# Optimization experiments

Measured on AMD Instinct MI355X. Metric: run time of the kernel, lower is better.

The kernel has to match this reference:

```python
import jax, jax.numpy as jnp
import numpy as np

NEG_POS_RATIO = 3
LOC_LOSS_ALPHA = 1.0
B, N, C = 64, 8732, 21  # batch, total prior boxes (SSD300), classes (VOC)


def setup_inputs() -> dict:
    key = jax.random.key(0)
    kd, km, kl, kpd, kpl = jax.random.split(key, 5)
    pos_mask = jax.random.bernoulli(km, 0.02, (B, N))
    actual_bbox_deltas = jax.random.normal(kd, (B, N, 4), dtype=jnp.float32) * pos_mask[..., None]
    cls = jax.random.randint(kl, (B, N), 0, C)
    actual_labels = jax.nn.one_hot(cls, C, dtype=jnp.float32)
    pred_bbox_deltas = jax.random.normal(kpd, (B, N, 4), dtype=jnp.float32)
    pred_labels = jax.random.normal(kpl, (B, N, C), dtype=jnp.float32)
    return {
        "actual_bbox_deltas": actual_bbox_deltas,
        "actual_labels": actual_labels,
        "pred_bbox_deltas": pred_bbox_deltas,
        "pred_labels": pred_labels,
    }


def reference(actual_bbox_deltas, actual_labels, pred_bbox_deltas, pred_labels):
    # positive boxes: any nonzero delta
    pos_cond = jnp.any(actual_bbox_deltas != 0, axis=2)          # [B, N] bool
    pos_count = jnp.sum(pos_cond, axis=1)                         # [B]
    neg_count = pos_count * NEG_POS_RATIO                         # [B]

    # CE from logits, used only to rank negatives for hard-negative mining
    ce_logits = -jnp.sum(actual_labels * jax.nn.log_softmax(pred_labels, axis=-1), axis=-1)  # [B, N]
    masked_loss = jnp.where(pos_cond, -jnp.inf, ce_logits)
    # rank[b, n] = position of box n in descending sort of masked_loss[b]
    order = jnp.argsort(-masked_loss, axis=1)
    rank = jnp.argsort(order, axis=1)
    neg_mask = rank < neg_count[:, None]                          # hardest negatives
    sel_mask = pos_cond | neg_mask                                # boxes entering conf loss

    total_pos = jnp.maximum(jnp.sum(pos_count), 1).astype(jnp.float32)

    # Huber (delta=1): TF Huber takes mean over last axis, then reduction='sum'
    d = pred_bbox_deltas - actual_bbox_deltas
    ad = jnp.abs(d)
    hub = jnp.where(ad <= 1.0, 0.5 * d * d, ad - 0.5)             # [B, N, 4]
    loc_loss = jnp.sum(jnp.mean(hub, axis=-1) * pos_cond) * LOC_LOSS_ALPHA

    # conf loss: TF CategoricalCrossentropy with from_logits=False (as in the original code,
    # applied to the raw pred_labels): normalize to sum 1, clip to epsilon, -sum(y*log p)
    eps = 1e-7
    p = pred_labels / jnp.sum(pred_labels, axis=-1, keepdims=True)
    p = jnp.clip(p, eps, 1.0 - eps)
    ce_probs = -jnp.sum(actual_labels * jnp.log(p), axis=-1)      # [B, N]
    conf_loss = jnp.sum(ce_probs * sel_mask)

    return loc_loss / total_pos, conf_loss / total_pos
```

## Files before the change

kernel.cpp:

```cpp
#include <hip/hip_runtime.h>
#include <math.h>

#define BB 64
#define NN 8732
#define NV4 (NN / 4)
#define CC 21
#define TB 256
#define GX 35

static __device__ __forceinline__ unsigned f2u(float f) {
  unsigned u = __float_as_uint(f);
  return (u & 0x80000000u) ? ~u : (u | 0x80000000u);
}

__global__ __launch_bounds__(256) void k1_map(
    const float* __restrict__ abd, const float* __restrict__ lbl,
    const float* __restrict__ pbd, const float* __restrict__ plog,
    unsigned* __restrict__ keys, float* __restrict__ cep,
    float* __restrict__ pl, float* __restrict__ pc, int* __restrict__ pcnt) {
  __shared__ float s_plog[TB * CC];
  __shared__ int s_cls[TB];
  __shared__ float s_l[4], s_p[4];
  __shared__ int s_c[4];

  const int b = blockIdx.y;
  const int base = blockIdx.x * TB;
  const int nbox = min(TB, NN - base);
  const int nf4 = (nbox * CC) / 4;
  const int tid = threadIdx.x;

  const float4* pl4 = reinterpret_cast<const float4*>(plog + ((size_t)b * NN + base) * CC);
  for (int t = tid; t < nf4; t += 256) {
    reinterpret_cast<float4*>(s_plog)[t] = pl4[t];
  }
  const float4* lb4 = reinterpret_cast<const float4*>(lbl + ((size_t)b * NN + base) * CC);
  for (int t = tid; t < nf4; t += 256) {
    float4 v = lb4[t];
    const unsigned f0 = (unsigned)t * 4u;
    if (v.x != 0.f) s_cls[(f0 + 0) / CC] = (int)((f0 + 0) % CC);
    if (v.y != 0.f) s_cls[(f0 + 1) / CC] = (int)((f0 + 1) % CC);
    if (v.z != 0.f) s_cls[(f0 + 2) / CC] = (int)((f0 + 2) % CC);
    if (v.w != 0.f) s_cls[(f0 + 3) / CC] = (int)((f0 + 3) % CC);
  }
  __syncthreads();

  const int n = base + tid;
  const bool valid = (tid < nbox);
  float loc = 0.f, pconf = 0.f;
  int isPos = 0;
  if (valid) {
    const size_t idx = (size_t)b * NN + n;
    const float4 a = reinterpret_cast<const float4*>(abd)[idx];
    const float4 p = reinterpret_cast<const float4*>(pbd)[idx];
    isPos = (a.x != 0.f) || (a.y != 0.f) || (a.z != 0.f) || (a.w != 0.f);

    const int cls = s_cls[tid];
    float pv[CC];
    float m = -INFINITY, ssum = 0.f, tdot = 0.f;
#pragma unroll
    for (int j = 0; j < CC; ++j) {
      const float v = s_plog[tid * CC + j];
      pv[j] = v;
      m = fmaxf(m, v);
      ssum += v;
      tdot = (j == cls) ? v : tdot;
    }
    float es = 0.f;
#pragma unroll
    for (int j = 0; j < CC; ++j) es += expf(pv[j] - m);
    float pt = tdot / ssum;
    float ptc = fminf(fmaxf(pt, 1e-7f), 1.0f - 1e-7f);
    float cp = -logf(ptc);
    float cel = (m + logf(es)) - tdot;
    keys[idx] = isPos ? 0u : f2u(cel);
    cep[idx] = cp;
    pconf = isPos ? cp : 0.f;
    float dx = p.x - a.x, dy = p.y - a.y, dz = p.z - a.z, dw = p.w - a.w;
    float axv = fabsf(dx), ayv = fabsf(dy), azv = fabsf(dz), awv = fabsf(dw);
    float h = (axv <= 1.f ? 0.5f * dx * dx : axv - 0.5f)
            + (ayv <= 1.f ? 0.5f * dy * dy : ayv - 0.5f)
            + (azv <= 1.f ? 0.5f * dz * dz : azv - 0.5f)
            + (awv <= 1.f ? 0.5f * dw * dw : awv - 0.5f);
    loc = isPos ? h * 0.25f : 0.f;
  }
  float lv = loc, pcf = pconf;
  int pctr = isPos;
  for (int off = 32; off > 0; off >>= 1) {
    lv += __shfl_down(lv, off, 64);
    pcf += __shfl_down(pcf, off, 64);
    pctr += __shfl_down(pctr, off, 64);
  }
  const int lane = tid & 63, wv = tid >> 6;
  if (lane == 0) { s_l[wv] = lv; s_p[wv] = pcf; s_c[wv] = pctr; }
  __syncthreads();
  if (tid == 0) {
    const int bi = b * GX + blockIdx.x;
    pl[bi] = s_l[0] + s_l[1] + s_l[2] + s_l[3];
    pc[bi] = s_p[0] + s_p[1] + s_p[2] + s_p[3];
    pcnt[bi] = s_c[0] + s_c[1] + s_c[2] + s_c[3];
  }
}

#define K2T 1024
#define K2W 16

__global__ __launch_bounds__(K2T) void k2_select(
    const unsigned* __restrict__ keys, const float* __restrict__ cep,
    const float* __restrict__ pl, const float* __restrict__ pc,
    const int* __restrict__ pcnt,
    double* __restrict__ row_loc, double* __restrict__ row_conf,
    int* __restrict__ row_pos) {
  __shared__ unsigned hist[2048];
  __shared__ unsigned wsum[K2W];
  __shared__ unsigned bc[2];
  __shared__ unsigned wtot[K2W];
  __shared__ double s_d[K2W];
  __shared__ double s_rl, s_rc;
  __shared__ int s_pos;
  const int b = blockIdx.x;
  const int tid = threadIdx.x;
  const int lane = tid & 63, wv = tid >> 6;

  if (wv == 0) {
    float a = 0.f, c = 0.f;
    int p = 0;
    if (lane < GX) {
      a = pl[b * GX + lane];
      c = pc[b * GX + lane];
      p = pcnt[b * GX + lane];
    }
    for (int off = 32; off > 0; off >>= 1) {
      a += __shfl_down(a, off, 64);
      c += __shfl_down(c, off, 64);
      p += __shfl_down(p, off, 64);
    }
    if (lane == 0) { s_rl = (double)a; s_rc = (double)c; s_pos = p; }
  }
  __syncthreads();
  const int pos = s_pos;
  unsigned k = (unsigned)(pos * 3);
  const unsigned negs = (unsigned)(NN - pos);
  if (k > negs) k = negs;

  double neg_total = 0.0;
  if (k > 0) {
    const unsigned* rk = keys + (size_t)b * NN;
    const uint4* rk4 = reinterpret_cast<const uint4*>(rk);
    unsigned want = k;
    unsigned prefix = 0;
    for (int pass = 0; pass < 3; ++pass) {
      const int nb = (pass == 2) ? 1024 : 2048;
      const int shift = (pass == 0) ? 21 : (pass == 1) ? 10 : 0;
      for (int i = tid; i < nb; i += K2T) hist[i] = 0;
      __syncthreads();
      if (pass == 0) {
        for (int t = tid; t < NV4; t += K2T) {
          uint4 v = rk4[t];
          atomicAdd(&hist[v.x >> 21], 1u);
          atomicAdd(&hist[v.y >> 21], 1u);
          atomicAdd(&hist[v.z >> 21], 1u);
          atomicAdd(&hist[v.w >> 21], 1u);
        }
      } else {
        const unsigned pshift = (pass == 1) ? 21u : 10u;
        const unsigned msk = (unsigned)(nb - 1);
        for (int t = tid; t < NV4; t += K2T) {
          uint4 v = rk4[t];
          if ((v.x >> pshift) == prefix) atomicAdd(&hist[(v.x >> shift) & msk], 1u);
          if ((v.y >> pshift) == prefix) atomicAdd(&hist[(v.y >> shift) & msk], 1u);
          if ((v.z >> pshift) == prefix) atomicAdd(&hist[(v.z >> shift) & msk], 1u);
          if ((v.w >> pshift) == prefix) atomicAdd(&hist[(v.w >> shift) & msk], 1u);
        }
      }
      __syncthreads();
      const int PR = nb / K2T;
      unsigned v0, v1 = 0, ls;
      if (PR == 2) {
        v0 = hist[nb - 1 - (tid * 2)];
        v1 = hist[nb - 1 - (tid * 2 + 1)];
        ls = v0 + v1;
      } else {
        v0 = hist[nb - 1 - tid];
        ls = v0;
      }
      unsigned x = ls;
#pragma unroll
      for (int off = 1; off < 64; off <<= 1) {
        unsigned y = __shfl_up(x, off, 64);
        if (lane >= off) x += y;
      }
      if (lane == 63) wsum[wv] = x;
      __syncthreads();
      if (wv == 0 && lane < K2W) {
        unsigned wx = wsum[lane];
#pragma unroll
        for (int off = 1; off < K2W; off <<= 1) {
          unsigned wy = __shfl_up(wx, off, K2W);
          if ((lane & (K2W - 1)) >= off) wx += wy;
        }
        wsum[lane] = wx;
      }
      __syncthreads();
      const unsigned woff = (wv == 0) ? 0u : wsum[wv - 1];
      const unsigned pinc = woff + x;
      if (PR == 2) {
        const unsigned p0 = pinc - ls + v0;
        const unsigned p1 = pinc;
        if (v0 > 0 && p0 >= want && p0 - v0 < want) { bc[0] = (unsigned)(nb - 1 - tid * 2); bc[1] = want - (p0 - v0); }
        if (v1 > 0 && p1 >= want && p1 - v1 < want) { bc[0] = (unsigned)(nb - 1 - (tid * 2 + 1)); bc[1] = want - (p1 - v1); }
      } else {
        if (v0 > 0 && pinc >= want && pinc - v0 < want) { bc[0] = (unsigned)(nb - 1 - tid); bc[1] = want - (pinc - v0); }
      }
      __syncthreads();
      const unsigned d = bc[0];
      want = bc[1];
      prefix = (pass == 0) ? d : ((prefix << ((pass == 1) ? 11 : 10)) | d);
      __syncthreads();
    }
    const unsigned tau = prefix;
    const unsigned neq = want;

    const float* rc = cep + (size_t)b * NN;
    double mysum = 0.0;
    unsigned bbase = 0;
    for (int start = 0; start < NN; start += K2T) {
      const int i = start + tid;
      const unsigned key = (i < NN) ? rk[i] : 0u;
      const bool gt = (i < NN) && (key > tau);
      const bool eq = (i < NN) && (key == tau);
      if (gt) mysum += (double)rc[i];
      const unsigned long long mb = __ballot(eq);
      if (lane == 0) wtot[wv] = (unsigned)__popcll(mb);
      __syncthreads();
      unsigned wpref = 0, tot = 0;
#pragma unroll
      for (int w = 0; w < K2W; ++w) {
        const unsigned c = wtot[w];
        wpref += (w < wv) ? c : 0u;
        tot += c;
      }
      if (eq) {
        const unsigned lanepref = (unsigned)__popcll(mb & ((1ull << lane) - 1ull));
        if (bbase + wpref + lanepref < neq) mysum += (double)rc[i];
      }
      bbase += tot;
      __syncthreads();
    }
    for (int off = 32; off > 0; off >>= 1) mysum += __shfl_down(mysum, off, 64);
    if (lane == 0) s_d[wv] = mysum;
    __syncthreads();
    if (tid == 0) {
#pragma unroll
      for (int w = 0; w < K2W; ++w) neg_total += s_d[w];
    }
  }
  if (tid == 0) {
    row_loc[b] = s_rl;
    row_conf[b] = s_rc + neg_total;
    row_pos[b] = pos;
  }
}

__global__ void k3_final(const double* __restrict__ row_loc,
                         const double* __restrict__ row_conf,
                         const int* __restrict__ row_pos,
                         float* __restrict__ out) {
  const int lane = threadIdx.x;
  double l = row_loc[lane], c = row_conf[lane];
  int p = row_pos[lane];
  for (int off = 32; off > 0; off >>= 1) {
    l += __shfl_down(l, off, 64);
    c += __shfl_down(c, off, 64);
    p += __shfl_down(p, off, 64);
  }
  if (lane == 0) {
    const double tot = (p > 0) ? (double)p : 1.0;
    out[0] = (float)(l / tot);
    out[1] = (float)(c / tot);
  }
}

extern "C" void kernel_launch(void* const* d_in, const int* in_sizes, int n_in,
                              void* d_out, int out_size, void* d_ws, size_t ws_size,
                              hipStream_t stream) {
  const float* abd = (const float*)d_in[0];
  const float* lbl = (const float*)d_in[1];
  const float* pbd = (const float*)d_in[2];
  const float* plog = (const float*)d_in[3];

  char* ws = (char*)d_ws;
  float* pl = (float*)(ws + 0);
  float* pc = (float*)(ws + 8960);
  int* pcnt = (int*)(ws + 17920);
  double* row_loc = (double*)(ws + 26880);
  double* row_conf = (double*)(ws + 27392);
  int* row_pos = (int*)(ws + 27904);
  unsigned* keys = (unsigned*)(ws + 28160);
  float* cep = (float*)(ws + 28160 + (size_t)BB * NN * sizeof(unsigned));

  dim3 g1(GX, BB);
  k1_map<<<g1, 256, 0, stream>>>(abd, lbl, pbd, plog, keys, cep, pl, pc, pcnt);
  k2_select<<<BB, K2T, 0, stream>>>(keys, cep, pl, pc, pcnt, row_loc, row_conf, row_pos);
  k3_final<<<1, 64, 0, stream>>>(row_loc, row_conf, row_pos, (float*)d_out);
}
```

Measured before the change: 44.37 us.

## Load logits directly into LDS and batch label/delta loads ahead of use

Replaces the register-staged copy of logits into shared memory with the global_load_lds builtin, so data moves straight from global memory to LDS. Label loads are unrolled into six register-held float4s, and the bbox delta loads are issued before the barrier so all global reads are in flight together. The class-index scan replaces per-element divide/modulo with incremental counters. In exchange it raises register pressure and depends on the LDS address layout matching the builtin's per-wave write semantics, which is easy to get wrong.

```diff
diff --git a/kernel.cpp b/kernel.cpp
--- a/kernel.cpp
+++ b/kernel.cpp
@@ -8,6 +8,10 @@
 #define TB 256
 #define GX 35
 
+typedef unsigned int u32;
+typedef __attribute__((address_space(1))) const u32 gu32;
+typedef __attribute__((address_space(3))) u32 lu32;
+
 static __device__ __forceinline__ unsigned f2u(float f) {
   unsigned u = __float_as_uint(f);
   return (u & 0x80000000u) ? ~u : (u | 0x80000000u);
@@ -18,7 +22,7 @@
     const float* __restrict__ pbd, const float* __restrict__ plog,
     unsigned* __restrict__ keys, float* __restrict__ cep,
     float* __restrict__ pl, float* __restrict__ pc, int* __restrict__ pcnt) {
-  __shared__ float s_plog[TB * CC];
+  __shared__ __align__(16) float s_plog[TB * CC];
   __shared__ int s_cls[TB];
   __shared__ float s_l[4], s_p[4];
   __shared__ int s_c[4];
@@ -26,32 +30,58 @@
   const int b = blockIdx.y;
   const int base = blockIdx.x * TB;
   const int nbox = min(TB, NN - base);
-  const int nf4 = (nbox * CC) / 4;
+  const int nf4 = (nbox * CC) >> 2;
   const int tid = threadIdx.x;
+  const int lane = tid & 63, wv = tid >> 6;
 
   const float4* pl4 = reinterpret_cast<const float4*>(plog + ((size_t)b * NN + base) * CC);
-  for (int t = tid; t < nf4; t += 256) {
-    reinterpret_cast<float4*>(s_plog)[t] = pl4[t];
-  }
+#pragma unroll
+  for (int it = 0; it < 6; ++it) {
+    const int t = it * 256 + tid;
+    if (t < nf4) {
+      __builtin_amdgcn_global_load_lds(
+          (gu32*)(const u32*)(pl4 + t),
+          (lu32*)(u32*)((char*)s_plog + ((size_t)(it * 256 + (tid & 0xC0))) * 16),
+          16, 0, 0);
+    }
+  }
+
   const float4* lb4 = reinterpret_cast<const float4*>(lbl + ((size_t)b * NN + base) * CC);
-  for (int t = tid; t < nf4; t += 256) {
-    float4 v = lb4[t];
-    const unsigned f0 = (unsigned)t * 4u;
-    if (v.x != 0.f) s_cls[(f0 + 0) / CC] = (int)((f0 + 0) % CC);
-    if (v.y != 0.f) s_cls[(f0 + 1) / CC] = (int)((f0 + 1) % CC);
-    if (v.z != 0.f) s_cls[(f0 + 2) / CC] = (int)((f0 + 2) % CC);
-    if (v.w != 0.f) s_cls[(f0 + 3) / CC] = (int)((f0 + 3) % CC);
+  float4 lv4[6];
+#pragma unroll
+  for (int it = 0; it < 6; ++it) {
+    const int t = it * 256 + tid;
+    lv4[it] = lb4[(t < nf4) ? t : (nf4 - 1)];
+  }
+  const int nclamp = base + ((tid < nbox) ? tid : (nbox - 1));
+  const size_t idxc = (size_t)b * NN + nclamp;
+  const float4 a = reinterpret_cast<const float4*>(abd)[idxc];
+  const float4 p = reinterpret_cast<const float4*>(pbd)[idxc];
+
+#pragma unroll
+  for (int it = 0; it < 6; ++it) {
+    const int t = it * 256 + tid;
+    if (t < nf4) {
+      const float4 v = lv4[it];
+      const int f0 = t * 4;
+      int box = f0 / CC;
+      int rem = f0 - box * CC;
+      if (v.x != 0.f) s_cls[box] = rem;
+      if (++rem == CC) { rem = 0; ++box; }
+      if (v.y != 0.f) s_cls[box] = rem;
+      if (++rem == CC) { rem = 0; ++box; }
+      if (v.z != 0.f) s_cls[box] = rem;
+      if (++rem == CC) { rem = 0; ++box; }
+      if (v.w != 0.f) s_cls[box] = rem;
+    }
   }
   __syncthreads();
 
-  const int n = base + tid;
   const bool valid = (tid < nbox);
   float loc = 0.f, pconf = 0.f;
   int isPos = 0;
   if (valid) {
-    const size_t idx = (size_t)b * NN + n;
-    const float4 a = reinterpret_cast<const float4*>(abd)[idx];
-    const float4 p = reinterpret_cast<const float4*>(pbd)[idx];
+    const size_t idx = (size_t)b * NN + base + tid;
     isPos = (a.x != 0.f) || (a.y != 0.f) || (a.z != 0.f) || (a.w != 0.f);
 
     const int cls = s_cls[tid];
@@ -83,15 +113,14 @@
             + (awv <= 1.f ? 0.5f * dw * dw : awv - 0.5f);
     loc = isPos ? h * 0.25f : 0.f;
   }
-  float lv = loc, pcf = pconf;
+  float lvv = loc, pcf = pconf;
   int pctr = isPos;
   for (int off = 32; off > 0; off >>= 1) {
-    lv += __shfl_down(lv, off, 64);
+    lvv += __shfl_down(lvv, off, 64);
     pcf += __shfl_down(pcf, off, 64);
     pctr += __shfl_down(pctr, off, 64);
   }
-  const int lane = tid & 63, wv = tid >> 6;
-  if (lane == 0) { s_l[wv] = lv; s_p[wv] = pcf; s_c[wv] = pctr; }
+  if (lane == 0) { s_l[wv] = lvv; s_p[wv] = pcf; s_c[wv] = pctr; }
   __syncthreads();
   if (tid == 0) {
     const int bi = b * GX + blockIdx.x;
```

Result: faster. 42.73 us (-3.7%).
